# Kernel optimization log

Measured on AMD Instinct MI355X. Metric: run time of the kernel, lower is better.

Reference implementation:

```python
import jax, jax.numpy as jnp
import numpy as np

B, S, HID = 1, 2048, 2048
H, HKV, D = 16, 8, 128

def _rope_tables(seq_len, dim, base=10000.0):
    inv_freq = 1.0 / (base ** (np.arange(0, dim, 2, dtype=np.float32) / dim))
    t = np.arange(seq_len, dtype=np.float32)
    freqs = np.outer(t, inv_freq)                      # [S, D/2]
    emb = np.concatenate([freqs, freqs], axis=-1)      # [S, D]
    return jnp.asarray(np.cos(emb)), jnp.asarray(np.sin(emb))

def setup_inputs() -> dict:
    key = jax.random.key(0)
    ks = jax.random.split(key, 5)
    x = jax.random.normal(ks[0], (B, S, HID), dtype=jnp.float32)
    Wq = jax.random.normal(ks[1], (H * D, HID), dtype=jnp.float32) * (HID ** -0.5)
    Wk = jax.random.normal(ks[2], (HKV * D, HID), dtype=jnp.float32) * (HID ** -0.5)
    Wv = jax.random.normal(ks[3], (HKV * D, HID), dtype=jnp.float32) * (HID ** -0.5)
    Wo = jax.random.normal(ks[4], (HID, H * D), dtype=jnp.float32) * ((H * D) ** -0.5)
    cos, sin = _rope_tables(S, D)
    return {"x": x, "Wq": Wq, "Wk": Wk, "Wv": Wv, "Wo": Wo, "cos": cos, "sin": sin}

def _rotate_half(t):
    t1, t2 = jnp.split(t, 2, axis=-1)
    return jnp.concatenate([-t2, t1], axis=-1)

def _apply_rope(t, cos, sin):
    # t: [B, h, S, D]; cos/sin: [S, D]
    return t * cos[None, None, :, :] + _rotate_half(t) * sin[None, None, :, :]

def reference(x, Wq, Wk, Wv, Wo, cos, sin):
    b, s, _ = x.shape
    # QKV projections (no bias) + shape to [B, h, S, D]
    q = jnp.einsum('bsh,eh->bse', x, Wq).reshape(b, s, H, D).transpose(0, 2, 1, 3)
    k = jnp.einsum('bsh,eh->bse', x, Wk).reshape(b, s, HKV, D).transpose(0, 2, 1, 3)
    v = jnp.einsum('bsh,eh->bse', x, Wv).reshape(b, s, HKV, D).transpose(0, 2, 1, 3)
    # rotary embedding (rotate-half, non-interleaved)
    q = _apply_rope(q, cos, sin)
    k = _apply_rope(k, cos, sin)
    # GQA: repeat kv heads to match query heads
    rep = H // HKV
    k = jnp.repeat(k, rep, axis=1)
    v = jnp.repeat(v, rep, axis=1)
    scale = D ** -0.5  # attn_scaling is None -> default 1/sqrt(dim_per_head)
    scores = jnp.einsum('bhqd,bhkd->bhqk', q, k) * scale
    causal = jnp.tril(jnp.ones((s, s), dtype=bool))  # decoder causal mask
    scores = jnp.where(causal[None, None, :, :], scores, jnp.finfo(scores.dtype).min)
    attn = jax.nn.softmax(scores, axis=-1)
    ctx = jnp.einsum('bhqk,bhkd->bhqd', attn, v)
    ctx = ctx.transpose(0, 2, 1, 3).reshape(b, s, H * D)  # unshape
    out = jnp.einsum('bse,he->bsh', ctx, Wo)  # final linear, no bias
    return out
```

## Files before the change

### kernel.cpp

```cpp
#include <hip/hip_runtime.h>
#include <hip/hip_bf16.h>

#define S_LEN 2048
#define HIDN  2048
#define NH    16
#define NKV   8
#define DH    128

typedef __bf16 bf16_t;
typedef __bf16 bf16x4 __attribute__((ext_vector_type(4)));
typedef __bf16 bf16x8 __attribute__((ext_vector_type(8)));
typedef float  floatx4 __attribute__((ext_vector_type(4)));

#define NEG_BIG (-1.0e30f)

#define BM 128
#define BN 128
#define BK 64

__device__ __forceinline__ void g2l16(const bf16_t* g, bf16_t* l) {
  __builtin_amdgcn_global_load_lds(
      (const __attribute__((address_space(1))) unsigned int*)g,
      (__attribute__((address_space(3))) unsigned int*)l, 16, 0, 0);
}

__global__ void cvt_all_kernel(const float* __restrict__ x,  const float* __restrict__ wq,
                               const float* __restrict__ wk, const float* __restrict__ wv,
                               const float* __restrict__ wo,
                               bf16_t* __restrict__ xc,  bf16_t* __restrict__ wqc,
                               bf16_t* __restrict__ wkc, bf16_t* __restrict__ wvc,
                               bf16_t* __restrict__ woc)
{
  const int b = blockIdx.x;
  const float* src; bf16_t* dst; int off;
  if      (b < 1024) { src = x;  dst = xc;  off = b; }
  else if (b < 2048) { src = wq; dst = wqc; off = b - 1024; }
  else if (b < 2560) { src = wk; dst = wkc; off = b - 2048; }
  else if (b < 3072) { src = wv; dst = wvc; off = b - 2560; }
  else               { src = wo; dst = woc; off = b - 3072; }
  const int base = off * 4096 + threadIdx.x;
  #pragma unroll
  for (int i = 0; i < 16; ++i)
    dst[base + i * 256] = (bf16_t)src[base + i * 256];
}

__device__ __forceinline__ void gemm_tile(
    const bf16_t* __restrict__ A, const bf16_t* __restrict__ Bt,
    int K, int m0, int n0, floatx4 acc[4][4], bf16_t* As, bf16_t* Bs)
{
  const int tid  = threadIdx.x;
  const int lane = tid & 63;
  const int wave = tid >> 6;
  const int wm = (wave & 1) << 6;
  const int wn = (wave >> 1) << 6;
  const int lr = lane & 15;
  const int lq = lane >> 4;

  #pragma unroll
  for (int i = 0; i < 4; ++i)
    #pragma unroll
    for (int j = 0; j < 4; ++j)
      acc[i][j] = floatx4{0.f, 0.f, 0.f, 0.f};

  for (int k0 = 0; k0 < K; k0 += BK) {
    #pragma unroll
    for (int it = 0; it < 4; ++it) {
      int linear = it * 256 + tid;
      int row = linear >> 3;
      int pc  = linear & 7;
      int c   = pc ^ (row & 7);
      g2l16(A  + (size_t)(m0 + row) * K + k0 + c * 8, As + linear * 8);
      g2l16(Bt + (size_t)(n0 + row) * K + k0 + c * 8, Bs + linear * 8);
    }
    __syncthreads();
    #pragma unroll
    for (int kk = 0; kk < BK; kk += 32) {
      bf16x8 af[4], bfr[4];
      #pragma unroll
      for (int t = 0; t < 4; ++t) {
        int pcr = ((kk >> 3) + lq) ^ (lr & 7);
        af[t]  = *(const bf16x8*)(As + (wm + t * 16 + lr) * BK + pcr * 8);
        bfr[t] = *(const bf16x8*)(Bs + (wn + t * 16 + lr) * BK + pcr * 8);
      }
      #pragma unroll
      for (int i = 0; i < 4; ++i)
        #pragma unroll
        for (int j = 0; j < 4; ++j)
          acc[i][j] = __builtin_amdgcn_mfma_f32_16x16x32_bf16(af[i], bfr[j], acc[i][j], 0, 0, 0);
    }
    __syncthreads();
  }
}

__global__ void __launch_bounds__(256, 2) gemm_qkv_kernel(
    const bf16_t* __restrict__ x, const bf16_t* __restrict__ Wq,
    const bf16_t* __restrict__ Wk, const bf16_t* __restrict__ Wv,
    bf16_t* __restrict__ qb, bf16_t* __restrict__ kb, bf16_t* __restrict__ vtb,
    const float* __restrict__ cosT, const float* __restrict__ sinT)
{
  __shared__ __align__(16) bf16_t As[BM * BK];
  __shared__ __align__(16) bf16_t Bs[BN * BK];
  __shared__ __align__(16) bf16_t Epi[128 * 132];
  const int tid = threadIdx.x;
  const int m0 = blockIdx.x * BM;
  const int nt = blockIdx.y;
  const bf16_t* Bt;
  int hbase;
  if (nt < 16)      { Bt = Wq + (size_t)nt * 128 * HIDN;        hbase = nt; }
  else if (nt < 24) { Bt = Wk + (size_t)(nt - 16) * 128 * HIDN; hbase = nt - 16; }
  else              { Bt = Wv + (size_t)(nt - 24) * 128 * HIDN; hbase = nt - 24; }

  floatx4 acc[4][4];
  gemm_tile(x, Bt, HIDN, m0, 0, acc, As, Bs);

  const int lane = tid & 63, wave = tid >> 6;
  const int wm = (wave & 1) << 6, wn = (wave >> 1) << 6;
  const int lr = lane & 15, lq = lane >> 4;
  #pragma unroll
  for (int i = 0; i < 4; ++i)
    #pragma unroll
    for (int j = 0; j < 4; ++j)
      #pragma unroll
      for (int r = 0; r < 4; ++r) {
        int row = wm + i * 16 + lq * 4 + r;
        int col = wn + j * 16 + lr;
        Epi[row * 132 + col] = (bf16_t)acc[i][j][r];
      }
  __syncthreads();

  if (nt < 24) {
    bf16_t* outp = (nt < 16) ? qb : kb;
    #pragma unroll
    for (int u = 0; u < 32; ++u) {
      int idx = u * 256 + tid;
      int dd = idx & 63, s = idx >> 6;
      float a = (float)Epi[s * 132 + dd];
      float b = (float)Epi[s * 132 + dd + 64];
      int sg = m0 + s;
      float cv = cosT[sg * DH + dd];
      float sv = sinT[sg * DH + dd];
      size_t off = ((size_t)hbase * S_LEN + sg) * DH;
      outp[off + dd]      = (bf16_t)(a * cv - b * sv);
      outp[off + dd + 64] = (bf16_t)(b * cv + a * sv);
    }
  } else {
    bf16_t* dst = vtb + (size_t)hbase * DH * S_LEN;
    #pragma unroll
    for (int u = 0; u < 64; ++u) {
      int idx = u * 256 + tid;
      int sl = idx & 127, d = idx >> 7;
      dst[(size_t)d * S_LEN + m0 + sl] = Epi[sl * 132 + d];
    }
  }
}

__global__ void __launch_bounds__(256, 2) gemm_out_kernel(
    const bf16_t* __restrict__ ctx, const bf16_t* __restrict__ Wo,
    float* __restrict__ out)
{
  __shared__ __align__(16) bf16_t As[BM * BK];
  __shared__ __align__(16) bf16_t Bs[BN * BK];
  const int m0 = blockIdx.x * BM;
  const int n0 = blockIdx.y * BN;
  floatx4 acc[4][4];
  gemm_tile(ctx, Wo, HIDN, m0, n0, acc, As, Bs);

  const int lane = threadIdx.x & 63, wave = threadIdx.x >> 6;
  const int wm = (wave & 1) << 6, wn = (wave >> 1) << 6;
  const int lr = lane & 15, lq = lane >> 4;
  #pragma unroll
  for (int i = 0; i < 4; ++i)
    #pragma unroll
    for (int j = 0; j < 4; ++j)
      #pragma unroll
      for (int r = 0; r < 4; ++r) {
        int srow = m0 + wm + i * 16 + lq * 4 + r;
        int col  = n0 + wn + j * 16 + lr;
        out[(size_t)srow * HIDN + col] = acc[i][j][r];
      }
}

__global__ void __launch_bounds__(256, 2) attn_kernel(
    const bf16_t* __restrict__ qb, const bf16_t* __restrict__ kb,
    const bf16_t* __restrict__ vtb, bf16_t* __restrict__ ctx)
{
  __shared__ __align__(16) bf16_t Kb[2][64 * 128];
  __shared__ __align__(16) bf16_t Vb[2][128 * 64];
  __shared__ __align__(16) bf16_t Pb[4][16 * 64];

  const int tid  = threadIdx.x;
  const int lane = tid & 63, wave = tid >> 6;
  const int lr   = lane & 15, quad = lane >> 4;

  const int b = blockIdx.x;
  int h, qt;
  if (b < 256) { h = b >> 5;              qt = b & 31; }
  else         { int c = b - 256; h = 8 + (c >> 5); qt = 31 - (c & 31); }
  const int hkv = h >> 1;
  const int q0  = qt * 64;
  const int nch = qt + 1;
  const int qrow_g = q0 + wave * 16 + lr;

  const bf16_t* kbase  = kb  + (size_t)hkv * S_LEN * DH;
  const bf16_t* vtbase = vtb + (size_t)hkv * DH * S_LEN;
  const float scale = 0.08838834764831845f;
  bf16_t* pmine = &Pb[wave][0];

  const bf16_t* qrp = qb + ((size_t)h * S_LEN + qrow_g) * DH;
  bf16x8 qf[4];
  #pragma unroll
  for (int kk = 0; kk < 4; ++kk)
    qf[kk] = *(const bf16x8*)(qrp + kk * 32 + quad * 8);

  auto stage = [&](int cc, int buf) {
    const int kv0 = cc * 64;
    #pragma unroll
    for (int it = 0; it < 4; ++it) {
      int linear = it * 256 + tid;
      int krow = linear >> 4, kpc = linear & 15;
      int kc = kpc ^ (krow & 15);
      g2l16(kbase + (size_t)(kv0 + krow) * DH + kc * 8, &Kb[buf][linear * 8]);
      int vrow = linear >> 3, vpc = linear & 7;
      int vc = vpc ^ (vrow & 7);
      g2l16(vtbase + (size_t)vrow * S_LEN + kv0 + vc * 8, &Vb[buf][linear * 8]);
    }
  };

  float m_r = NEG_BIG, l_r = 0.f;
  floatx4 o[8];
  #pragma unroll
  for (int t = 0; t < 8; ++t) o[t] = floatx4{0.f, 0.f, 0.f, 0.f};

  stage(0, 0);

  for (int cc = 0; cc < nch; ++cc) {
    const int buf = cc & 1;
    __syncthreads();
    if (cc + 1 < nch) stage(cc + 1, buf ^ 1);
    const int kv0 = cc * 64;

    floatx4 sacc[4];
    #pragma unroll
    for (int t = 0; t < 4; ++t) sacc[t] = floatx4{0.f, 0.f, 0.f, 0.f};
    #pragma unroll
    for (int kk = 0; kk < 4; ++kk) {
      const int pc = ((kk << 2) + quad) ^ lr;
      #pragma unroll
      for (int t = 0; t < 4; ++t) {
        bf16x8 kf = *(const bf16x8*)(&Kb[buf][(t * 16 + lr) * 128 + pc * 8]);
        sacc[t] = __builtin_amdgcn_mfma_f32_16x16x32_bf16(kf, qf[kk], sacc[t], 0, 0, 0);
      }
    }

    if (cc == nch - 1) {
      #pragma unroll
      for (int t = 0; t < 4; ++t)
        #pragma unroll
        for (int r = 0; r < 4; ++r) {
          int kv = kv0 + t * 16 + quad * 4 + r;
          if (kv > qrow_g) sacc[t][r] = NEG_BIG;
        }
    }

    float mx = sacc[0][0];
    #pragma unroll
    for (int t = 0; t < 4; ++t)
      #pragma unroll
      for (int r = 0; r < 4; ++r) mx = fmaxf(mx, sacc[t][r]);
    mx = fmaxf(mx, __shfl_xor(mx, 16, 64));
    mx = fmaxf(mx, __shfl_xor(mx, 32, 64));
    const float mn = fmaxf(m_r, mx * scale);
    const float alpha = __expf(m_r - mn);

    float lc = 0.f;
    #pragma unroll
    for (int t = 0; t < 4; ++t) {
      bf16x4 pk;
      #pragma unroll
      for (int r = 0; r < 4; ++r) {
        float p = __expf(fmaf(sacc[t][r], scale, -mn));
        lc += p;
        pk[r] = (bf16_t)p;
      }
      int pw = lr * 64 + (((2 * t + (quad >> 1)) ^ (lr & 7)) << 3) + (quad & 1) * 4;
      *(bf16x4*)(pmine + pw) = pk;
    }
    lc += __shfl_xor(lc, 16, 64);
    lc += __shfl_xor(lc, 32, 64);
    l_r = l_r * alpha + lc;
    m_r = mn;

    #pragma unroll
    for (int t = 0; t < 8; ++t)
      #pragma unroll
      for (int r = 0; r < 4; ++r) o[t][r] *= alpha;
    #pragma unroll
    for (int ks = 0; ks < 2; ++ks) {
      int prd = lr * 64 + (((ks * 4 + quad) ^ (lr & 7)) << 3);
      bf16x8 pf = *(const bf16x8*)(pmine + prd);
      #pragma unroll
      for (int t = 0; t < 8; ++t) {
        int pc = (ks * 4 + quad) ^ (lr & 7);
        bf16x8 vf = *(const bf16x8*)(&Vb[buf][(t * 16 + lr) * 64 + pc * 8]);
        o[t] = __builtin_amdgcn_mfma_f32_16x16x32_bf16(vf, pf, o[t], 0, 0, 0);
      }
    }
  }

  const float inv = 1.0f / l_r;
  bf16_t* crow = ctx + (size_t)qrow_g * HIDN + h * DH;
  #pragma unroll
  for (int t = 0; t < 8; ++t) {
    bf16x4 ov;
    #pragma unroll
    for (int r = 0; r < 4; ++r) ov[r] = (bf16_t)(o[t][r] * inv);
    *(bf16x4*)(crow + t * 16 + quad * 4) = ov;
  }
}

extern "C" void kernel_launch(void* const* d_in, const int* in_sizes, int n_in,
                              void* d_out, int out_size, void* d_ws, size_t ws_size,
                              hipStream_t stream)
{
  const float* xf   = (const float*)d_in[0];
  const float* Wqf  = (const float*)d_in[1];
  const float* Wkf  = (const float*)d_in[2];
  const float* Wvf  = (const float*)d_in[3];
  const float* Wof  = (const float*)d_in[4];
  const float* cosT = (const float*)d_in[5];
  const float* sinT = (const float*)d_in[6];
  float* out = (float*)d_out;

  char* ws = (char*)d_ws;
  const size_t MB = 1u << 20;
  bf16_t* xc  = (bf16_t*)(ws);
  bf16_t* Wqc = (bf16_t*)(ws + 8  * MB);
  bf16_t* Wkc = (bf16_t*)(ws + 16 * MB);
  bf16_t* Wvc = (bf16_t*)(ws + 20 * MB);
  bf16_t* Woc = (bf16_t*)(ws + 24 * MB);
  bf16_t* qb  = (bf16_t*)(ws + 32 * MB);
  bf16_t* kb  = (bf16_t*)(ws + 40 * MB);
  bf16_t* vtb = (bf16_t*)(ws + 44 * MB);
  bf16_t* ctx = (bf16_t*)(ws + 48 * MB);

  hipLaunchKernelGGL(cvt_all_kernel, dim3(4096), dim3(256), 0, stream,
                     xf, Wqf, Wkf, Wvf, Wof, xc, Wqc, Wkc, Wvc, Woc);
  hipLaunchKernelGGL(gemm_qkv_kernel, dim3(16, 32), dim3(256), 0, stream,
                     xc, Wqc, Wkc, Wvc, qb, kb, vtb, cosT, sinT);
  hipLaunchKernelGGL(attn_kernel, dim3(512), dim3(256), 0, stream,
                     qb, kb, vtb, ctx);
  hipLaunchKernelGGL(gemm_out_kernel, dim3(16, 16), dim3(256), 0, stream,
                     ctx, Woc, out);
}
```

Baseline: 237.9 us.

## Fuse fp32-to-bf16 conversion into GEMM loads and share KV across GQA heads

Removes the separate conversion kernel. The QKV and output GEMMs now load fp32 operands into registers, convert them to bf16 and store them into double-buffered shared memory, prefetching the next K slice while the current one is computed. The attention kernel is remapped so each block handles both query heads of one KV head over 32 query rows, so K/V tiles staged in LDS are reused by two heads. This saves a full pass over the weights and activations, but it doubles the fp32 bytes read per GEMM tile and gives up the asynchronous global-to-LDS path for converted operands.

```diff
diff --git a/kernel.cpp b/kernel.cpp
--- a/kernel.cpp
+++ b/kernel.cpp
@@ -17,6 +17,7 @@
 #define BM 128
 #define BN 128
 #define BK 64
+#define TILE (BM * BK)
 
 __device__ __forceinline__ void g2l16(const bf16_t* g, bf16_t* l) {
   __builtin_amdgcn_global_load_lds(
@@ -24,28 +25,8 @@
       (__attribute__((address_space(3))) unsigned int*)l, 16, 0, 0);
 }
 
-__global__ void cvt_all_kernel(const float* __restrict__ x,  const float* __restrict__ wq,
-                               const float* __restrict__ wk, const float* __restrict__ wv,
-                               const float* __restrict__ wo,
-                               bf16_t* __restrict__ xc,  bf16_t* __restrict__ wqc,
-                               bf16_t* __restrict__ wkc, bf16_t* __restrict__ wvc,
-                               bf16_t* __restrict__ woc)
-{
-  const int b = blockIdx.x;
-  const float* src; bf16_t* dst; int off;
-  if      (b < 1024) { src = x;  dst = xc;  off = b; }
-  else if (b < 2048) { src = wq; dst = wqc; off = b - 1024; }
-  else if (b < 2560) { src = wk; dst = wkc; off = b - 2048; }
-  else if (b < 3072) { src = wv; dst = wvc; off = b - 2560; }
-  else               { src = wo; dst = woc; off = b - 3072; }
-  const int base = off * 4096 + threadIdx.x;
-  #pragma unroll
-  for (int i = 0; i < 16; ++i)
-    dst[base + i * 256] = (bf16_t)src[base + i * 256];
-}
-
-__device__ __forceinline__ void gemm_tile(
-    const bf16_t* __restrict__ A, const bf16_t* __restrict__ Bt,
+__device__ __forceinline__ void gemm_tile_f32(
+    const float* __restrict__ A, const float* __restrict__ Bt,
     int K, int m0, int n0, floatx4 acc[4][4], bf16_t* As, bf16_t* Bs)
 {
   const int tid  = threadIdx.x;
@@ -62,25 +43,56 @@
     for (int j = 0; j < 4; ++j)
       acc[i][j] = floatx4{0.f, 0.f, 0.f, 0.f};
 
-  for (int k0 = 0; k0 < K; k0 += BK) {
+  floatx4 ra[4][2], rb[4][2];
+  auto ld = [&](int k0) {
     #pragma unroll
     for (int it = 0; it < 4; ++it) {
       int linear = it * 256 + tid;
       int row = linear >> 3;
       int pc  = linear & 7;
       int c   = pc ^ (row & 7);
-      g2l16(A  + (size_t)(m0 + row) * K + k0 + c * 8, As + linear * 8);
-      g2l16(Bt + (size_t)(n0 + row) * K + k0 + c * 8, Bs + linear * 8);
-    }
+      const float* pa = A  + (size_t)(m0 + row) * K + k0 + c * 8;
+      const float* pb = Bt + (size_t)(n0 + row) * K + k0 + c * 8;
+      ra[it][0] = *(const floatx4*)(pa);
+      ra[it][1] = *(const floatx4*)(pa + 4);
+      rb[it][0] = *(const floatx4*)(pb);
+      rb[it][1] = *(const floatx4*)(pb + 4);
+    }
+  };
+  auto st = [&](int buf) {
+    #pragma unroll
+    for (int it = 0; it < 4; ++it) {
+      int linear = it * 256 + tid;
+      bf16x8 va, vb;
+      #pragma unroll
+      for (int j = 0; j < 4; ++j) {
+        va[j]     = (bf16_t)ra[it][0][j];
+        va[4 + j] = (bf16_t)ra[it][1][j];
+        vb[j]     = (bf16_t)rb[it][0][j];
+        vb[4 + j] = (bf16_t)rb[it][1][j];
+      }
+      *(bf16x8*)(As + buf * TILE + linear * 8) = va;
+      *(bf16x8*)(Bs + buf * TILE + linear * 8) = vb;
+    }
+  };
+
+  ld(0);
+  int kidx = 0;
+  for (int k0 = 0; k0 < K; k0 += BK, ++kidx) {
+    const int buf = kidx & 1;
+    st(buf);
     __syncthreads();
+    if (k0 + BK < K) ld(k0 + BK);
+    const bf16_t* Ab = As + buf * TILE;
+    const bf16_t* Bb = Bs + buf * TILE;
     #pragma unroll
     for (int kk = 0; kk < BK; kk += 32) {
       bf16x8 af[4], bfr[4];
       #pragma unroll
       for (int t = 0; t < 4; ++t) {
         int pcr = ((kk >> 3) + lq) ^ (lr & 7);
-        af[t]  = *(const bf16x8*)(As + (wm + t * 16 + lr) * BK + pcr * 8);
-        bfr[t] = *(const bf16x8*)(Bs + (wn + t * 16 + lr) * BK + pcr * 8);
+        af[t]  = *(const bf16x8*)(Ab + (wm + t * 16 + lr) * BK + pcr * 8);
+        bfr[t] = *(const bf16x8*)(Bb + (wn + t * 16 + lr) * BK + pcr * 8);
       }
       #pragma unroll
       for (int i = 0; i < 4; ++i)
@@ -88,31 +100,31 @@
         for (int j = 0; j < 4; ++j)
           acc[i][j] = __builtin_amdgcn_mfma_f32_16x16x32_bf16(af[i], bfr[j], acc[i][j], 0, 0, 0);
     }
-    __syncthreads();
   }
 }
 
 __global__ void __launch_bounds__(256, 2) gemm_qkv_kernel(
-    const bf16_t* __restrict__ x, const bf16_t* __restrict__ Wq,
-    const bf16_t* __restrict__ Wk, const bf16_t* __restrict__ Wv,
+    const float* __restrict__ x, const float* __restrict__ Wq,
+    const float* __restrict__ Wk, const float* __restrict__ Wv,
     bf16_t* __restrict__ qb, bf16_t* __restrict__ kb, bf16_t* __restrict__ vtb,
     const float* __restrict__ cosT, const float* __restrict__ sinT)
 {
-  __shared__ __align__(16) bf16_t As[BM * BK];
-  __shared__ __align__(16) bf16_t Bs[BN * BK];
-  __shared__ __align__(16) bf16_t Epi[128 * 132];
+  __shared__ __align__(16) bf16_t As[2 * TILE];
+  __shared__ __align__(16) bf16_t Bs[2 * TILE];
   const int tid = threadIdx.x;
   const int m0 = blockIdx.x * BM;
   const int nt = blockIdx.y;
-  const bf16_t* Bt;
+  const float* Bt;
   int hbase;
   if (nt < 16)      { Bt = Wq + (size_t)nt * 128 * HIDN;        hbase = nt; }
   else if (nt < 24) { Bt = Wk + (size_t)(nt - 16) * 128 * HIDN; hbase = nt - 16; }
   else              { Bt = Wv + (size_t)(nt - 24) * 128 * HIDN; hbase = nt - 24; }
 
   floatx4 acc[4][4];
-  gemm_tile(x, Bt, HIDN, m0, 0, acc, As, Bs);
-
+  gemm_tile_f32(x, Bt, HIDN, m0, 0, acc, As, Bs);
+
+  __syncthreads();
+  bf16_t* Epi = As;
   const int lane = tid & 63, wave = tid >> 6;
   const int wm = (wave & 1) << 6, wn = (wave >> 1) << 6;
   const int lr = lane & 15, lq = lane >> 4;
@@ -124,7 +136,7 @@
       for (int r = 0; r < 4; ++r) {
         int row = wm + i * 16 + lq * 4 + r;
         int col = wn + j * 16 + lr;
-        Epi[row * 132 + col] = (bf16_t)acc[i][j][r];
+        Epi[row * 128 + col] = (bf16_t)acc[i][j][r];
       }
   __syncthreads();
 
@@ -134,8 +146,8 @@
     for (int u = 0; u < 32; ++u) {
       int idx = u * 256 + tid;
       int dd = idx & 63, s = idx >> 6;
-      float a = (float)Epi[s * 132 + dd];
-      float b = (float)Epi[s * 132 + dd + 64];
+      float a = (float)Epi[s * 128 + dd];
+      float b = (float)Epi[s * 128 + dd + 64];
       int sg = m0 + s;
       float cv = cosT[sg * DH + dd];
       float sv = sinT[sg * DH + dd];
@@ -149,25 +161,83 @@
     for (int u = 0; u < 64; ++u) {
       int idx = u * 256 + tid;
       int sl = idx & 127, d = idx >> 7;
-      dst[(size_t)d * S_LEN + m0 + sl] = Epi[sl * 132 + d];
+      dst[(size_t)d * S_LEN + m0 + sl] = Epi[sl * 128 + d];
     }
   }
 }
 
 __global__ void __launch_bounds__(256, 2) gemm_out_kernel(
-    const bf16_t* __restrict__ ctx, const bf16_t* __restrict__ Wo,
+    const bf16_t* __restrict__ ctx, const float* __restrict__ Wo,
     float* __restrict__ out)
 {
-  __shared__ __align__(16) bf16_t As[BM * BK];
-  __shared__ __align__(16) bf16_t Bs[BN * BK];
+  __shared__ __align__(16) bf16_t As[2 * TILE];
+  __shared__ __align__(16) bf16_t Bs[2 * TILE];
+  const int tid = threadIdx.x;
+  const int lane = tid & 63, wave = tid >> 6;
+  const int wm = (wave & 1) << 6, wn = (wave >> 1) << 6;
+  const int lr = lane & 15, lq = lane >> 4;
   const int m0 = blockIdx.x * BM;
   const int n0 = blockIdx.y * BN;
+
   floatx4 acc[4][4];
-  gemm_tile(ctx, Wo, HIDN, m0, n0, acc, As, Bs);
-
-  const int lane = threadIdx.x & 63, wave = threadIdx.x >> 6;
-  const int wm = (wave & 1) << 6, wn = (wave >> 1) << 6;
-  const int lr = lane & 15, lq = lane >> 4;
+  #pragma unroll
+  for (int i = 0; i < 4; ++i)
+    #pragma unroll
+    for (int j = 0; j < 4; ++j)
+      acc[i][j] = floatx4{0.f, 0.f, 0.f, 0.f};
+
+  floatx4 rb[4][2];
+  auto ldb = [&](int k0) {
+    #pragma unroll
+    for (int it = 0; it < 4; ++it) {
+      int linear = it * 256 + tid;
+      int row = linear >> 3, pc = linear & 7;
+      int c = pc ^ (row & 7);
+      const float* pb = Wo + (size_t)(n0 + row) * HIDN + k0 + c * 8;
+      rb[it][0] = *(const floatx4*)(pb);
+      rb[it][1] = *(const floatx4*)(pb + 4);
+    }
+  };
+
+  ldb(0);
+  int kidx = 0;
+  for (int k0 = 0; k0 < HIDN; k0 += BK, ++kidx) {
+    const int buf = kidx & 1;
+    #pragma unroll
+    for (int it = 0; it < 4; ++it) {
+      int linear = it * 256 + tid;
+      int row = linear >> 3, pc = linear & 7;
+      int c = pc ^ (row & 7);
+      bf16x8 vb;
+      #pragma unroll
+      for (int j = 0; j < 4; ++j) {
+        vb[j]     = (bf16_t)rb[it][0][j];
+        vb[4 + j] = (bf16_t)rb[it][1][j];
+      }
+      *(bf16x8*)(Bs + buf * TILE + linear * 8) = vb;
+      g2l16(ctx + (size_t)(m0 + row) * HIDN + k0 + c * 8, As + buf * TILE + linear * 8);
+    }
+    __syncthreads();
+    if (k0 + BK < HIDN) ldb(k0 + BK);
+    const bf16_t* Ab = As + buf * TILE;
+    const bf16_t* Bb = Bs + buf * TILE;
+    #pragma unroll
+    for (int kk = 0; kk < BK; kk += 32) {
+      bf16x8 af[4], bfr[4];
+      #pragma unroll
+      for (int t = 0; t < 4; ++t) {
+        int pcr = ((kk >> 3) + lq) ^ (lr & 7);
+        af[t]  = *(const bf16x8*)(Ab + (wm + t * 16 + lr) * BK + pcr * 8);
+        bfr[t] = *(const bf16x8*)(Bb + (wn + t * 16 + lr) * BK + pcr * 8);
+      }
+      #pragma unroll
+      for (int i = 0; i < 4; ++i)
+        #pragma unroll
+        for (int j = 0; j < 4; ++j)
+          acc[i][j] = __builtin_amdgcn_mfma_f32_16x16x32_bf16(af[i], bfr[j], acc[i][j], 0, 0, 0);
+    }
+  }
+
   #pragma unroll
   for (int i = 0; i < 4; ++i)
     #pragma unroll
@@ -193,20 +263,20 @@
   const int lr   = lane & 15, quad = lane >> 4;
 
   const int b = blockIdx.x;
-  int h, qt;
-  if (b < 256) { h = b >> 5;              qt = b & 31; }
-  else         { int c = b - 256; h = 8 + (c >> 5); qt = 31 - (c & 31); }
-  const int hkv = h >> 1;
-  const int q0  = qt * 64;
-  const int nch = qt + 1;
-  const int qrow_g = q0 + wave * 16 + lr;
+  int hkv, t32;
+  if (b < 256) { hkv = b >> 5; t32 = b & 31; }
+  else         { int c = b - 256; hkv = c >> 5; t32 = 63 - (c & 31); }
+  const int head = hkv * 2 + (wave >> 1);
+  const int q0   = t32 * 32;
+  const int nch  = (t32 >> 1) + 1;
+  const int qrow_g = q0 + ((wave & 1) << 4) + lr;
 
   const bf16_t* kbase  = kb  + (size_t)hkv * S_LEN * DH;
   const bf16_t* vtbase = vtb + (size_t)hkv * DH * S_LEN;
   const float scale = 0.08838834764831845f;
   bf16_t* pmine = &Pb[wave][0];
 
-  const bf16_t* qrp = qb + ((size_t)h * S_LEN + qrow_g) * DH;
+  const bf16_t* qrp = qb + ((size_t)head * S_LEN + qrow_g) * DH;
   bf16x8 qf[4];
   #pragma unroll
   for (int kk = 0; kk < 4; ++kk)
@@ -308,7 +378,7 @@
   }
 
   const float inv = 1.0f / l_r;
-  bf16_t* crow = ctx + (size_t)qrow_g * HIDN + h * DH;
+  bf16_t* crow = ctx + (size_t)qrow_g * HIDN + head * DH;
   #pragma unroll
   for (int t = 0; t < 8; ++t) {
     bf16x4 ov;
@@ -333,22 +403,15 @@
 
   char* ws = (char*)d_ws;
   const size_t MB = 1u << 20;
-  bf16_t* xc  = (bf16_t*)(ws);
-  bf16_t* Wqc = (bf16_t*)(ws + 8  * MB);
-  bf16_t* Wkc = (bf16_t*)(ws + 16 * MB);
-  bf16_t* Wvc = (bf16_t*)(ws + 20 * MB);
-  bf16_t* Woc = (bf16_t*)(ws + 24 * MB);
-  bf16_t* qb  = (bf16_t*)(ws + 32 * MB);
-  bf16_t* kb  = (bf16_t*)(ws + 40 * MB);
-  bf16_t* vtb = (bf16_t*)(ws + 44 * MB);
-  bf16_t* ctx = (bf16_t*)(ws + 48 * MB);
-
-  hipLaunchKernelGGL(cvt_all_kernel, dim3(4096), dim3(256), 0, stream,
-                     xf, Wqf, Wkf, Wvf, Wof, xc, Wqc, Wkc, Wvc, Woc);
+  bf16_t* qb  = (bf16_t*)(ws);
+  bf16_t* kb  = (bf16_t*)(ws + 8  * MB);
+  bf16_t* vtb = (bf16_t*)(ws + 12 * MB);
+  bf16_t* ctx = (bf16_t*)(ws + 16 * MB);
+
   hipLaunchKernelGGL(gemm_qkv_kernel, dim3(16, 32), dim3(256), 0, stream,
-                     xc, Wqc, Wkc, Wvc, qb, kb, vtb, cosT, sinT);
+                     xf, Wqf, Wkf, Wvf, qb, kb, vtb, cosT, sinT);
   hipLaunchKernelGGL(attn_kernel, dim3(512), dim3(256), 0, stream,
                      qb, kb, vtb, ctx);
   hipLaunchKernelGGL(gemm_out_kernel, dim3(16, 16), dim3(256), 0, stream,
-                     ctx, Woc, out);
-}
+                     ctx, Wof, out);
+}
```

After: 265.9 us. 1.12x slower.
